# Performance work log

Measured on AMD Instinct MI355X. Metric: run time of the kernel, lower is better.

Reference implementation:

```python
import jax, jax.numpy as jnp
import numpy as np

B, S, H, E, K, D = 1, 4096, 1024, 8, 2, 2048

def setup_inputs() -> dict:
    key = jax.random.key(0)
    k1, k2, k3, k4, k5 = jax.random.split(key, 5)
    x = jax.random.normal(k1, (B, S, H), dtype=jnp.float32)
    attention_mask = jnp.ones((B, S), dtype=jnp.int32)
    expert_weights = jax.random.uniform(k2, (B, S, K), dtype=jnp.float32)
    # distinct top-K expert indices per token (torch code requires at most one match per token)
    r = jax.random.uniform(k3, (B, S, E))
    chosen_expert_indices = jnp.argsort(r, axis=-1)[..., :K].astype(jnp.int64)
    down_proj = jax.random.normal(k4, (E, H, D), dtype=jnp.float32)
    up_proj = jax.random.normal(k5, (E, D, H), dtype=jnp.float32)
    return {"x": x, "attention_mask": attention_mask, "expert_weights": expert_weights,
            "chosen_expert_indices": chosen_expert_indices, "down_proj": down_proj, "up_proj": up_proj}

def reference(x, attention_mask, expert_weights, chosen_expert_indices, down_proj, up_proj):
    b, s, h = x.shape
    e = down_proj.shape[0]
    xt = x.reshape(-1, h)                                   # [N,H]
    n = xt.shape[0]
    mask = attention_mask.reshape(n, 1).astype(x.dtype)     # [N,1]
    idx = chosen_expert_indices.reshape(n, -1)              # [N,K]
    w = expert_weights.reshape(n, -1)                       # [N,K]
    onehot = jax.nn.one_hot(idx, e, dtype=x.dtype)          # [N,K,E]
    # per-token routing weight for each expert (0 if not chosen), masked
    we = jnp.einsum('nk,nke->ne', w, onehot) * mask         # [N,E]
    hid = jax.nn.relu(jnp.einsum('nh,ehd->end', xt, down_proj))  # [E,N,D]
    y = jnp.einsum('end,edh->enh', hid, up_proj)            # [E,N,H]
    mlp = jnp.einsum('ne,enh->nh', we, y)                   # [N,H]
    out = xt + mlp                                          # residual (B==1 as in source)
    return out.reshape(b, s, h)
```

## Files before the change

### kernel.cpp

```cpp
#include <hip/hip_runtime.h>
#include <stdint.h>

#define NTOK 4096
#define HDIM 1024
#define DDIM 2048
#define NEXP 8
#define NASS 8192

typedef __attribute__((ext_vector_type(8))) short bf16x8;
typedef __attribute__((ext_vector_type(4))) float f32x4;

typedef __attribute__((address_space(1))) const unsigned int gu32;
typedef __attribute__((address_space(3))) unsigned int lu32;

#define BARRIER() asm volatile("s_barrier" ::: "memory")

__device__ __forceinline__ void async16(void* lds, const void* g) {
  __builtin_amdgcn_global_load_lds((gu32*)(uintptr_t)g, (lu32*)(uintptr_t)lds, 16, 0, 0);
}

__device__ __forceinline__ unsigned short f2bf(float f) {
  unsigned int u = __float_as_uint(f);
  return (unsigned short)((u + 0x7fffu + ((u >> 16) & 1u)) >> 16);
}
__device__ __forceinline__ float bf2f(unsigned short u) {
  return __uint_as_float(((unsigned int)u) << 16);
}

__global__ __launch_bounds__(256) void k_cvt_x(const float* __restrict__ x,
                                               unsigned short* __restrict__ x16) {
  int i = blockIdx.x * 256 + threadIdx.x;
  float4 v = reinterpret_cast<const float4*>(x)[i];
  ushort4 o;
  o.x = f2bf(v.x); o.y = f2bf(v.y); o.z = f2bf(v.z); o.w = f2bf(v.w);
  reinterpret_cast<ushort4*>(x16)[i] = o;
}

__global__ __launch_bounds__(256) void k_transpose(const float* __restrict__ in,
                                                   unsigned short* __restrict__ out,
                                                   int R, int C) {
  __shared__ float t[32][33];
  const size_t mbase = (size_t)blockIdx.z * R * C;
  int tid = threadIdx.x;
  int r = tid >> 3, c4 = (tid & 7) * 4;
  int gr = blockIdx.y * 32 + r;
  int gc = blockIdx.x * 32 + c4;
  float4 v = *reinterpret_cast<const float4*>(in + mbase + (size_t)gr * C + gc);
  t[r][c4 + 0] = v.x; t[r][c4 + 1] = v.y; t[r][c4 + 2] = v.z; t[r][c4 + 3] = v.w;
  __syncthreads();
  int orow = blockIdx.x * 32 + r;
  int oc4  = blockIdx.y * 32 + c4;
  ushort4 o;
  o.x = f2bf(t[c4 + 0][r]); o.y = f2bf(t[c4 + 1][r]);
  o.z = f2bf(t[c4 + 2][r]); o.w = f2bf(t[c4 + 3][r]);
  *reinterpret_cast<ushort4*>(out + mbase + (size_t)orow * R + oc4) = o;
}

__global__ __launch_bounds__(1024) void k_route(
    const int* __restrict__ idx, const float* __restrict__ ew,
    const int* __restrict__ amask,
    int* __restrict__ counts_g, int* __restrict__ offs_g,
    int* __restrict__ toks, float* __restrict__ wl, int* __restrict__ slotmap) {
  __shared__ int cnt[NEXP], cur[NEXP], flag;
  const int t = threadIdx.x;
  if (t < NEXP) cnt[t] = 0;
  if (t == 0) flag = 0;
  __syncthreads();
  int lf = 0;
#pragma unroll
  for (int j = 0; j < 4; ++j) {
    int i = t + j * 1024;
    if (idx[2 * i + 1] != 0) lf = 1;
  }
  if (lf) atomicOr(&flag, 1);
  __syncthreads();
  const int is32 = flag;
  int e[8];
#pragma unroll
  for (int j = 0; j < 8; ++j) {
    int i = t + j * 1024;
    int ei = is32 ? idx[i] : idx[2 * i];
    e[j] = ei;
    atomicAdd(&cnt[ei], 1);
  }
  __syncthreads();
  if (t == 0) {
    int off = 0;
    for (int k = 0; k < NEXP; ++k) {
      cur[k] = off; offs_g[k] = off; counts_g[k] = cnt[k]; off += cnt[k];
    }
  }
  __syncthreads();
#pragma unroll
  for (int j = 0; j < 8; ++j) {
    int i = t + j * 1024;
    int n = i >> 1;
    int slot = atomicAdd(&cur[e[j]], 1);
    toks[slot] = n;
    wl[slot] = ew[i] * (amask[n] ? 1.0f : 0.0f);
    slotmap[i] = slot;
  }
}

__global__ __launch_bounds__(512, 4) void k_gemm_down(
    const unsigned short* __restrict__ x16, const unsigned short* __restrict__ bT,
    const int* __restrict__ counts, const int* __restrict__ offs,
    const int* __restrict__ toks, unsigned short* __restrict__ hid) {
  const int e = blockIdx.x;
  const int cnt = counts[e];
  const int q = blockIdx.y;
  const int mt = q >> 4;
  const int nt = q & 15;
  if (mt * 128 >= cnt) return;
  const int base = offs[e];
  __shared__ alignas(16) char lds[65536];
  const int tid = threadIdx.x;
  const int lane = tid & 63;
  const int wr = ((tid >> 8) & 1) * 64;
  const int wc = ((tid >> 6) & 3) * 32;

  const char* gA[2]; const char* gB[2]; int sOff[2];
  {
    const int swcol = ((tid & 7) << 4) ^ (((tid >> 3) & 7) << 4);
#pragma unroll
    for (int it = 0; it < 2; ++it) {
      int row = it * 64 + (tid >> 3);
      int sl = mt * 128 + row; if (sl >= cnt) sl = cnt - 1;
      gA[it] = (const char*)(x16 + (size_t)toks[base + sl] * HDIM) + swcol;
      gB[it] = (const char*)(bT + (size_t)e * DDIM * HDIM + (size_t)(nt * 128 + row) * HDIM) + swcol;
      sOff[it] = it * 8192 + tid * 16;
    }
  }
  const int swz = (lane & 7) << 4;
  const int lo = (lane >> 4) << 4;
  int rowA[4], rowB[2];
#pragma unroll
  for (int m = 0; m < 4; ++m) rowA[m] = (wr + m * 16 + (lane & 15)) * 128;
#pragma unroll
  for (int n = 0; n < 2; ++n) rowB[n] = (wc + n * 16 + (lane & 15)) * 128;

#pragma unroll
  for (int it = 0; it < 2; ++it) {
    async16(lds + sOff[it], gA[it]);
    async16(lds + 32768 + sOff[it], gB[it]);
  }
  asm volatile("s_waitcnt vmcnt(0)" ::: "memory");
  BARRIER();

  f32x4 acc[4][2] = {};
  for (int j = 0; j < 16; ++j) {
    char* curA = lds + ((j & 1) << 14);
    char* curB = lds + 32768 + ((j & 1) << 14);
    char* nxtA = lds + ((~j & 1) << 14);
    char* nxtB = lds + 32768 + ((~j & 1) << 14);
    bf16x8 fa[4], fb[2];
    {
      const int cx = lo ^ swz;
#pragma unroll
      for (int m = 0; m < 4; ++m) fa[m] = *reinterpret_cast<const bf16x8*>(curA + rowA[m] + cx);
#pragma unroll
      for (int n = 0; n < 2; ++n) fb[n] = *reinterpret_cast<const bf16x8*>(curB + rowB[n] + cx);
    }
    if (j < 15) {
      const int ko = (j + 1) << 7;
#pragma unroll
      for (int it = 0; it < 2; ++it) {
        async16(nxtA + sOff[it], gA[it] + ko);
        async16(nxtB + sOff[it], gB[it] + ko);
      }
    }
    BARRIER();
    asm volatile("s_waitcnt lgkmcnt(0)" ::: "memory");
    __builtin_amdgcn_sched_barrier(0);
    __builtin_amdgcn_s_setprio(1);
#pragma unroll
    for (int m = 0; m < 4; ++m)
#pragma unroll
      for (int n = 0; n < 2; ++n)
        acc[m][n] = __builtin_amdgcn_mfma_f32_16x16x32_bf16(fa[m], fb[n], acc[m][n], 0, 0, 0);
    __builtin_amdgcn_s_setprio(0);
    BARRIER();
    {
      const int cx = (64 | lo) ^ swz;
#pragma unroll
      for (int m = 0; m < 4; ++m) fa[m] = *reinterpret_cast<const bf16x8*>(curA + rowA[m] + cx);
#pragma unroll
      for (int n = 0; n < 2; ++n) fb[n] = *reinterpret_cast<const bf16x8*>(curB + rowB[n] + cx);
    }
    BARRIER();
    asm volatile("s_waitcnt lgkmcnt(0)" ::: "memory");
    __builtin_amdgcn_sched_barrier(0);
    __builtin_amdgcn_s_setprio(1);
#pragma unroll
    for (int m = 0; m < 4; ++m)
#pragma unroll
      for (int n = 0; n < 2; ++n)
        acc[m][n] = __builtin_amdgcn_mfma_f32_16x16x32_bf16(fa[m], fb[n], acc[m][n], 0, 0, 0);
    __builtin_amdgcn_s_setprio(0);
    asm volatile("s_waitcnt vmcnt(0)" ::: "memory");
    BARRIER();
  }

#pragma unroll
  for (int m = 0; m < 4; ++m) {
    int r0 = mt * 128 + wr + m * 16 + ((lane >> 4) * 4);
#pragma unroll
    for (int j = 0; j < 4; ++j) {
      int r = r0 + j;
      if (r < cnt) {
        unsigned short* dst = hid + (size_t)(base + r) * DDIM + nt * 128 + wc + (lane & 15);
#pragma unroll
        for (int n = 0; n < 2; ++n) {
          float v = acc[m][n][j];
          dst[n * 16] = f2bf(v > 0.f ? v : 0.f);
        }
      }
    }
  }
}

__global__ __launch_bounds__(512, 4) void k_gemm_up(
    const unsigned short* __restrict__ hid, const unsigned short* __restrict__ bT,
    const int* __restrict__ counts, const int* __restrict__ offs,
    unsigned short* __restrict__ yw) {
  const int e = blockIdx.x;
  const int cnt = counts[e];
  const int q = blockIdx.y;
  const int mt = q >> 3;
  const int nt = q & 7;
  if (mt * 128 >= cnt) return;
  const int base = offs[e];
  __shared__ alignas(16) char lds[65536];
  const int tid = threadIdx.x;
  const int lane = tid & 63;
  const int wr = ((tid >> 8) & 1) * 64;
  const int wc = ((tid >> 6) & 3) * 32;

  const char* gA[2]; const char* gB[2]; int sOff[2];
  {
    const int swcol = ((tid & 7) << 4) ^ (((tid >> 3) & 7) << 4);
#pragma unroll
    for (int it = 0; it < 2; ++it) {
      int row = it * 64 + (tid >> 3);
      int sl = mt * 128 + row; if (sl >= cnt) sl = cnt - 1;
      gA[it] = (const char*)(hid + (size_t)(base + sl) * DDIM) + swcol;
      gB[it] = (const char*)(bT + (size_t)e * HDIM * DDIM + (size_t)(nt * 128 + row) * DDIM) + swcol;
      sOff[it] = it * 8192 + tid * 16;
    }
  }
  const int swz = (lane & 7) << 4;
  const int lo = (lane >> 4) << 4;
  int rowA[4], rowB[2];
#pragma unroll
  for (int m = 0; m < 4; ++m) rowA[m] = (wr + m * 16 + (lane & 15)) * 128;
#pragma unroll
  for (int n = 0; n < 2; ++n) rowB[n] = (wc + n * 16 + (lane & 15)) * 128;

#pragma unroll
  for (int it = 0; it < 2; ++it) {
    async16(lds + sOff[it], gA[it]);
    async16(lds + 32768 + sOff[it], gB[it]);
  }
  asm volatile("s_waitcnt vmcnt(0)" ::: "memory");
  BARRIER();

  f32x4 acc[4][2] = {};
  for (int j = 0; j < 32; ++j) {
    char* curA = lds + ((j & 1) << 14);
    char* curB = lds + 32768 + ((j & 1) << 14);
    char* nxtA = lds + ((~j & 1) << 14);
    char* nxtB = lds + 32768 + ((~j & 1) << 14);
    bf16x8 fa[4], fb[2];
    {
      const int cx = lo ^ swz;
#pragma unroll
      for (int m = 0; m < 4; ++m) fa[m] = *reinterpret_cast<const bf16x8*>(curA + rowA[m] + cx);
#pragma unroll
      for (int n = 0; n < 2; ++n) fb[n] = *reinterpret_cast<const bf16x8*>(curB + rowB[n] + cx);
    }
    if (j < 31) {
      const int ko = (j + 1) << 7;
#pragma unroll
      for (int it = 0; it < 2; ++it) {
        async16(nxtA + sOff[it], gA[it] + ko);
        async16(nxtB + sOff[it], gB[it] + ko);
      }
    }
    BARRIER();
    asm volatile("s_waitcnt lgkmcnt(0)" ::: "memory");
    __builtin_amdgcn_sched_barrier(0);
    __builtin_amdgcn_s_setprio(1);
#pragma unroll
    for (int m = 0; m < 4; ++m)
#pragma unroll
      for (int n = 0; n < 2; ++n)
        acc[m][n] = __builtin_amdgcn_mfma_f32_16x16x32_bf16(fa[m], fb[n], acc[m][n], 0, 0, 0);
    __builtin_amdgcn_s_setprio(0);
    BARRIER();
    {
      const int cx = (64 | lo) ^ swz;
#pragma unroll
      for (int m = 0; m < 4; ++m) fa[m] = *reinterpret_cast<const bf16x8*>(curA + rowA[m] + cx);
#pragma unroll
      for (int n = 0; n < 2; ++n) fb[n] = *reinterpret_cast<const bf16x8*>(curB + rowB[n] + cx);
    }
    BARRIER();
    asm volatile("s_waitcnt lgkmcnt(0)" ::: "memory");
    __builtin_amdgcn_sched_barrier(0);
    __builtin_amdgcn_s_setprio(1);
#pragma unroll
    for (int m = 0; m < 4; ++m)
#pragma unroll
      for (int n = 0; n < 2; ++n)
        acc[m][n] = __builtin_amdgcn_mfma_f32_16x16x32_bf16(fa[m], fb[n], acc[m][n], 0, 0, 0);
    __builtin_amdgcn_s_setprio(0);
    asm volatile("s_waitcnt vmcnt(0)" ::: "memory");
    BARRIER();
  }

#pragma unroll
  for (int m = 0; m < 4; ++m) {
    int r0 = mt * 128 + wr + m * 16 + ((lane >> 4) * 4);
#pragma unroll
    for (int j = 0; j < 4; ++j) {
      int r = r0 + j;
      if (r < cnt) {
        unsigned short* dst = yw + (size_t)(base + r) * HDIM + nt * 128 + wc + (lane & 15);
#pragma unroll
        for (int n = 0; n < 2; ++n) dst[n * 16] = f2bf(acc[m][n][j]);
      }
    }
  }
}

__global__ __launch_bounds__(256) void k_combine(
    const float* __restrict__ x, const unsigned short* __restrict__ yw,
    const int* __restrict__ slotmap, const float* __restrict__ wl,
    float* __restrict__ out) {
  const int n = blockIdx.x;
  const int t = threadIdx.x;
  const int s0 = slotmap[2 * n], s1 = slotmap[2 * n + 1];
  const float w0 = wl[s0], w1 = wl[s1];
  float4 xv = reinterpret_cast<const float4*>(x + (size_t)n * HDIM)[t];
  ushort4 a0 = reinterpret_cast<const ushort4*>(yw + (size_t)s0 * HDIM)[t];
  ushort4 b0 = reinterpret_cast<const ushort4*>(yw + (size_t)s1 * HDIM)[t];
  float4 r;
  r.x = xv.x + w0 * bf2f(a0.x) + w1 * bf2f(b0.x);
  r.y = xv.y + w0 * bf2f(a0.y) + w1 * bf2f(b0.y);
  r.z = xv.z + w0 * bf2f(a0.z) + w1 * bf2f(b0.z);
  r.w = xv.w + w0 * bf2f(a0.w) + w1 * bf2f(b0.w);
  reinterpret_cast<float4*>(out + (size_t)n * HDIM)[t] = r;
}

extern "C" void kernel_launch(void* const* d_in, const int* in_sizes, int n_in,
                              void* d_out, int out_size, void* d_ws, size_t ws_size,
                              hipStream_t stream) {
  const float* x    = (const float*)d_in[0];
  const int* amask  = (const int*)d_in[1];
  const float* ew   = (const float*)d_in[2];
  const int* cidx   = (const int*)d_in[3];
  const float* dn   = (const float*)d_in[4];
  const float* up   = (const float*)d_in[5];
  float* out        = (float*)d_out;
  char* ws          = (char*)d_ws;

  const size_t X16_OFF = 0;
  const size_t DNT_OFF = X16_OFF + (size_t)NTOK * HDIM * 2;
  const size_t UPT_OFF = DNT_OFF + (size_t)NEXP * HDIM * DDIM * 2;
  const size_t HID_OFF = UPT_OFF + (size_t)NEXP * HDIM * DDIM * 2;
  const size_t MET_OFF = HID_OFF + (size_t)NASS * DDIM * 2;

  unsigned short* x16 = (unsigned short*)(ws + X16_OFF);
  unsigned short* dnT = (unsigned short*)(ws + DNT_OFF);
  unsigned short* upT = (unsigned short*)(ws + UPT_OFF);
  unsigned short* hid = (unsigned short*)(ws + HID_OFF);
  unsigned short* yw  = (unsigned short*)(ws + DNT_OFF);
  int* counts  = (int*)(ws + MET_OFF);
  int* offs    = counts + 8;
  int* toks    = counts + 32;
  float* wl    = (float*)(toks + NASS);
  int* slotmap = (int*)(wl + NASS);

  k_cvt_x<<<NTOK * HDIM / 1024, 256, 0, stream>>>(x, x16);
  k_transpose<<<dim3(DDIM / 32, HDIM / 32, NEXP), 256, 0, stream>>>(dn, dnT, HDIM, DDIM);
  k_transpose<<<dim3(HDIM / 32, DDIM / 32, NEXP), 256, 0, stream>>>(up, upT, DDIM, HDIM);
  k_route<<<1, 1024, 0, stream>>>(cidx, ew, amask, counts, offs, toks, wl, slotmap);
  k_gemm_down<<<dim3(8, 1024), 512, 0, stream>>>(x16, dnT, counts, offs, toks, hid);
  k_gemm_up<<<dim3(8, 512), 512, 0, stream>>>(hid, upT, counts, offs, yw);
  k_combine<<<NTOK, 256, 0, stream>>>(x, yw, slotmap, wl, out);
}
```

Baseline: 157.6 us.

## Fuse up-projection transpose into down GEMM launch and drop mid-iteration barriers

The separate transpose kernel for up_proj is removed. Its tiles are now handled by extra blocks (blockIdx.y >= 1024) of the down-projection GEMM launch, so the transpose work can overlap with GEMM blocks and one launch disappears. Both GEMM inner loops now load both k-halves of the LDS fragments up front and issue all MFMAs back to back. This drops two barriers, the lgkmcnt waits and the setprio hints per iteration, at the cost of more live registers. The transpose blocks only use 512 of the 2048 columns' worth of work mapping, so the grid sizing and the wait for upT before k_gemm_up both need to be correct.

```diff
diff --git a/kernel.cpp b/kernel.cpp
--- a/kernel.cpp
+++ b/kernel.cpp
@@ -14,6 +14,7 @@
 typedef __attribute__((address_space(3))) unsigned int lu32;
 
 #define BARRIER() asm volatile("s_barrier" ::: "memory")
+#define WAIT_VM0() asm volatile("s_waitcnt vmcnt(0)" ::: "memory")
 
 __device__ __forceinline__ void async16(void* lds, const void* g) {
   __builtin_amdgcn_global_load_lds((gu32*)(uintptr_t)g, (lu32*)(uintptr_t)lds, 16, 0, 0);
@@ -102,19 +103,44 @@
   }
 }
 
-__global__ __launch_bounds__(512, 4) void k_gemm_down(
+__global__ __launch_bounds__(512, 4) void k_down_fused(
     const unsigned short* __restrict__ x16, const unsigned short* __restrict__ bT,
     const int* __restrict__ counts, const int* __restrict__ offs,
-    const int* __restrict__ toks, unsigned short* __restrict__ hid) {
+    const int* __restrict__ toks, unsigned short* __restrict__ hid,
+    const float* __restrict__ up, unsigned short* __restrict__ upT) {
   const int e = blockIdx.x;
+  const int q = blockIdx.y;
+  const int tid = threadIdx.x;
+  __shared__ alignas(16) char lds[65536];
+
+  if (q >= 1024) {
+    const int tt = (q - 1024) * 2 + (tid >> 8);
+    const int bx = tt & 31;
+    const int by = tt >> 5;
+    float* tb = (float*)lds + (tid >> 8) * (32 * 33);
+    const int t2 = tid & 255;
+    const int r = t2 >> 3, c4 = (t2 & 7) * 4;
+    const size_t mbase = (size_t)e * DDIM * HDIM;
+    const int gr = by * 32 + r;
+    const int gc = bx * 32 + c4;
+    float4 v = *reinterpret_cast<const float4*>(up + mbase + (size_t)gr * HDIM + gc);
+    tb[r * 33 + c4 + 0] = v.x; tb[r * 33 + c4 + 1] = v.y;
+    tb[r * 33 + c4 + 2] = v.z; tb[r * 33 + c4 + 3] = v.w;
+    __syncthreads();
+    const int orow = bx * 32 + r;
+    const int oc4  = by * 32 + c4;
+    ushort4 o;
+    o.x = f2bf(tb[(c4 + 0) * 33 + r]); o.y = f2bf(tb[(c4 + 1) * 33 + r]);
+    o.z = f2bf(tb[(c4 + 2) * 33 + r]); o.w = f2bf(tb[(c4 + 3) * 33 + r]);
+    *reinterpret_cast<ushort4*>(upT + mbase + (size_t)orow * DDIM + oc4) = o;
+    return;
+  }
+
   const int cnt = counts[e];
-  const int q = blockIdx.y;
   const int mt = q >> 4;
   const int nt = q & 15;
   if (mt * 128 >= cnt) return;
   const int base = offs[e];
-  __shared__ alignas(16) char lds[65536];
-  const int tid = threadIdx.x;
   const int lane = tid & 63;
   const int wr = ((tid >> 8) & 1) * 64;
   const int wc = ((tid >> 6) & 3) * 32;
@@ -144,7 +170,7 @@
     async16(lds + sOff[it], gA[it]);
     async16(lds + 32768 + sOff[it], gB[it]);
   }
-  asm volatile("s_waitcnt vmcnt(0)" ::: "memory");
+  WAIT_VM0();
   BARRIER();
 
   f32x4 acc[4][2] = {};
@@ -153,13 +179,13 @@
     char* curB = lds + 32768 + ((j & 1) << 14);
     char* nxtA = lds + ((~j & 1) << 14);
     char* nxtB = lds + 32768 + ((~j & 1) << 14);
-    bf16x8 fa[4], fb[2];
+    bf16x8 fa0[4], fb0[2], fa1[4], fb1[2];
     {
       const int cx = lo ^ swz;
 #pragma unroll
-      for (int m = 0; m < 4; ++m) fa[m] = *reinterpret_cast<const bf16x8*>(curA + rowA[m] + cx);
-#pragma unroll
-      for (int n = 0; n < 2; ++n) fb[n] = *reinterpret_cast<const bf16x8*>(curB + rowB[n] + cx);
+      for (int m = 0; m < 4; ++m) fa0[m] = *reinterpret_cast<const bf16x8*>(curA + rowA[m] + cx);
+#pragma unroll
+      for (int n = 0; n < 2; ++n) fb0[n] = *reinterpret_cast<const bf16x8*>(curB + rowB[n] + cx);
     }
     if (j < 15) {
       const int ko = (j + 1) << 7;
@@ -169,35 +195,24 @@
         async16(nxtB + sOff[it], gB[it] + ko);
       }
     }
-    BARRIER();
-    asm volatile("s_waitcnt lgkmcnt(0)" ::: "memory");
-    __builtin_amdgcn_sched_barrier(0);
-    __builtin_amdgcn_s_setprio(1);
-#pragma unroll
-    for (int m = 0; m < 4; ++m)
-#pragma unroll
-      for (int n = 0; n < 2; ++n)
-        acc[m][n] = __builtin_amdgcn_mfma_f32_16x16x32_bf16(fa[m], fb[n], acc[m][n], 0, 0, 0);
-    __builtin_amdgcn_s_setprio(0);
-    BARRIER();
     {
       const int cx = (64 | lo) ^ swz;
 #pragma unroll
-      for (int m = 0; m < 4; ++m) fa[m] = *reinterpret_cast<const bf16x8*>(curA + rowA[m] + cx);
-#pragma unroll
-      for (int n = 0; n < 2; ++n) fb[n] = *reinterpret_cast<const bf16x8*>(curB + rowB[n] + cx);
-    }
-    BARRIER();
-    asm volatile("s_waitcnt lgkmcnt(0)" ::: "memory");
-    __builtin_amdgcn_sched_barrier(0);
-    __builtin_amdgcn_s_setprio(1);
+      for (int m = 0; m < 4; ++m) fa1[m] = *reinterpret_cast<const bf16x8*>(curA + rowA[m] + cx);
+#pragma unroll
+      for (int n = 0; n < 2; ++n) fb1[n] = *reinterpret_cast<const bf16x8*>(curB + rowB[n] + cx);
+    }
 #pragma unroll
     for (int m = 0; m < 4; ++m)
 #pragma unroll
       for (int n = 0; n < 2; ++n)
-        acc[m][n] = __builtin_amdgcn_mfma_f32_16x16x32_bf16(fa[m], fb[n], acc[m][n], 0, 0, 0);
-    __builtin_amdgcn_s_setprio(0);
-    asm volatile("s_waitcnt vmcnt(0)" ::: "memory");
+        acc[m][n] = __builtin_amdgcn_mfma_f32_16x16x32_bf16(fa0[m], fb0[n], acc[m][n], 0, 0, 0);
+#pragma unroll
+    for (int m = 0; m < 4; ++m)
+#pragma unroll
+      for (int n = 0; n < 2; ++n)
+        acc[m][n] = __builtin_amdgcn_mfma_f32_16x16x32_bf16(fa1[m], fb1[n], acc[m][n], 0, 0, 0);
+    WAIT_VM0();
     BARRIER();
   }
 
@@ -261,7 +276,7 @@
     async16(lds + sOff[it], gA[it]);
     async16(lds + 32768 + sOff[it], gB[it]);
   }
-  asm volatile("s_waitcnt vmcnt(0)" ::: "memory");
+  WAIT_VM0();
   BARRIER();
 
   f32x4 acc[4][2] = {};
@@ -270,13 +285,13 @@
     char* curB = lds + 32768 + ((j & 1) << 14);
     char* nxtA = lds + ((~j & 1) << 14);
     char* nxtB = lds + 32768 + ((~j & 1) << 14);
-    bf16x8 fa[4], fb[2];
+    bf16x8 fa0[4], fb0[2], fa1[4], fb1[2];
     {
       const int cx = lo ^ swz;
 #pragma unroll
-      for (int m = 0; m < 4; ++m) fa[m] = *reinterpret_cast<const bf16x8*>(curA + rowA[m] + cx);
-#pragma unroll
-      for (int n = 0; n < 2; ++n) fb[n] = *reinterpret_cast<const bf16x8*>(curB + rowB[n] + cx);
+      for (int m = 0; m < 4; ++m) fa0[m] = *reinterpret_cast<const bf16x8*>(curA + rowA[m] + cx);
+#pragma unroll
+      for (int n = 0; n < 2; ++n) fb0[n] = *reinterpret_cast<const bf16x8*>(curB + rowB[n] + cx);
     }
     if (j < 31) {
       const int ko = (j + 1) << 7;
@@ -286,35 +301,24 @@
         async16(nxtB + sOff[it], gB[it] + ko);
       }
     }
-    BARRIER();
-    asm volatile("s_waitcnt lgkmcnt(0)" ::: "memory");
-    __builtin_amdgcn_sched_barrier(0);
-    __builtin_amdgcn_s_setprio(1);
-#pragma unroll
-    for (int m = 0; m < 4; ++m)
-#pragma unroll
-      for (int n = 0; n < 2; ++n)
-        acc[m][n] = __builtin_amdgcn_mfma_f32_16x16x32_bf16(fa[m], fb[n], acc[m][n], 0, 0, 0);
-    __builtin_amdgcn_s_setprio(0);
-    BARRIER();
     {
       const int cx = (64 | lo) ^ swz;
 #pragma unroll
-      for (int m = 0; m < 4; ++m) fa[m] = *reinterpret_cast<const bf16x8*>(curA + rowA[m] + cx);
-#pragma unroll
-      for (int n = 0; n < 2; ++n) fb[n] = *reinterpret_cast<const bf16x8*>(curB + rowB[n] + cx);
-    }
-    BARRIER();
-    asm volatile("s_waitcnt lgkmcnt(0)" ::: "memory");
-    __builtin_amdgcn_sched_barrier(0);
-    __builtin_amdgcn_s_setprio(1);
+      for (int m = 0; m < 4; ++m) fa1[m] = *reinterpret_cast<const bf16x8*>(curA + rowA[m] + cx);
+#pragma unroll
+      for (int n = 0; n < 2; ++n) fb1[n] = *reinterpret_cast<const bf16x8*>(curB + rowB[n] + cx);
+    }
 #pragma unroll
     for (int m = 0; m < 4; ++m)
 #pragma unroll
       for (int n = 0; n < 2; ++n)
-        acc[m][n] = __builtin_amdgcn_mfma_f32_16x16x32_bf16(fa[m], fb[n], acc[m][n], 0, 0, 0);
-    __builtin_amdgcn_s_setprio(0);
-    asm volatile("s_waitcnt vmcnt(0)" ::: "memory");
+        acc[m][n] = __builtin_amdgcn_mfma_f32_16x16x32_bf16(fa0[m], fb0[n], acc[m][n], 0, 0, 0);
+#pragma unroll
+    for (int m = 0; m < 4; ++m)
+#pragma unroll
+      for (int n = 0; n < 2; ++n)
+        acc[m][n] = __builtin_amdgcn_mfma_f32_16x16x32_bf16(fa1[m], fb1[n], acc[m][n], 0, 0, 0);
+    WAIT_VM0();
     BARRIER();
   }
 
@@ -383,9 +387,9 @@
 
   k_cvt_x<<<NTOK * HDIM / 1024, 256, 0, stream>>>(x, x16);
   k_transpose<<<dim3(DDIM / 32, HDIM / 32, NEXP), 256, 0, stream>>>(dn, dnT, HDIM, DDIM);
-  k_transpose<<<dim3(HDIM / 32, DDIM / 32, NEXP), 256, 0, stream>>>(up, upT, DDIM, HDIM);
   k_route<<<1, 1024, 0, stream>>>(cidx, ew, amask, counts, offs, toks, wl, slotmap);
-  k_gemm_down<<<dim3(8, 1024), 512, 0, stream>>>(x16, dnT, counts, offs, toks, hid);
+  k_down_fused<<<dim3(8, 2048), 512, 0, stream>>>(x16, dnT, counts, offs, toks, hid,
+                                                  up, upT);
   k_gemm_up<<<dim3(8, 512), 512, 0, stream>>>(hid, upT, counts, offs, yw);
   k_combine<<<NTOK, 256, 0, stream>>>(x, yw, slotmap, wl, out);
 }
```

New measurement: 159.8 us. No clear change (+1.4%).
